# Performance work log

Measured on AMD Instinct MI355X. Metric: run time of the kernel, lower is better.

Reference implementation:

```python
import jax, jax.numpy as jnp
import numpy as np

N_NODES = 50000
N_EDGES = 800000
N_GRAPHS = 512
VOCAB = 128
HID = 64
NCLS = 5


def _seg_mean(vals, ids, num_segments):
    s = jax.ops.segment_sum(vals, ids, num_segments=num_segments)
    cnt = jax.ops.segment_sum(jnp.ones((vals.shape[0],), vals.dtype), ids, num_segments=num_segments)
    return s / jnp.maximum(cnt, 1.0)[:, None]


def sage_conv(x, src, dst, W_l, b_l, W_r):
    # PyG SAGEConv (mean aggr): out = lin_l(mean_{j in N(i)} x_j) + lin_r(x_i)
    agg = _seg_mean(x[src], dst, x.shape[0])          # [N, H] gather + scatter-mean
    return agg @ W_l.T + b_l + x @ W_r.T


def setup_inputs() -> dict:
    key = jax.random.key(0)
    ks = jax.random.split(key, 10)
    scale = 1.0 / np.sqrt(HID)
    x_tokens = jax.random.randint(ks[0], (N_NODES,), 0, VOCAB)
    edge_index = jax.random.randint(ks[1], (2, N_EDGES), 0, N_NODES)
    batch = jnp.sort(jax.random.randint(ks[2], (N_NODES,), 0, N_GRAPHS))
    return {
        "x_tokens": x_tokens,
        "edge_index": edge_index,
        "batch": batch,
        "embed": jax.random.normal(ks[3], (VOCAB, HID), jnp.float32),
        "W1l": jax.random.normal(ks[4], (HID, HID), jnp.float32) * scale,
        "b1l": jnp.zeros((HID,), jnp.float32),
        "W1r": jax.random.normal(ks[5], (HID, HID), jnp.float32) * scale,
        "W2l": jax.random.normal(ks[6], (HID, HID), jnp.float32) * scale,
        "b2l": jnp.zeros((HID,), jnp.float32),
        "W2r": jax.random.normal(ks[7], (HID, HID), jnp.float32) * scale,
        "Wlin": jax.random.normal(ks[8], (NCLS, HID), jnp.float32) * scale,
        "blin": jnp.zeros((NCLS,), jnp.float32),
    }


def reference(x_tokens, edge_index, batch, embed, W1l, b1l, W1r, W2l, b2l, W2r, Wlin, blin):
    src, dst = edge_index[0], edge_index[1]
    x = embed[x_tokens]                                  # [N, H] embedding lookup
    x = jax.nn.relu(sage_conv(x, src, dst, W1l, b1l, W1r))
    x = jax.nn.relu(sage_conv(x, src, dst, W2l, b2l, W2r))
    g = _seg_mean(x, batch, N_GRAPHS)                    # global_mean_pool -> [G, H]
    return g @ Wlin.T + blin                             # [G, num_classes]
```

## Files before the change

kernel.cpp:

```cpp
#include <hip/hip_runtime.h>

#define N_NODES  50000
#define N_EDGES  800000
#define N_GRAPHS 512
#define HID      64
#define NCLS     5
#define NB       64
#define EST      36
#define AST      68

typedef __attribute__((ext_vector_type(8))) short bf16x8;
typedef __attribute__((ext_vector_type(4))) float f32x4;

__device__ inline unsigned short f2bf(float f) {
    unsigned int u = __builtin_bit_cast(unsigned int, f);
    unsigned int r = (u + 0x7FFFu + ((u >> 16) & 1u)) >> 16;
    return (unsigned short)r;
}
__device__ inline unsigned int packbf(float a, float b) {
    return (unsigned int)f2bf(a) | ((unsigned int)f2bf(b) << 16);
}
__device__ inline float bf2f(unsigned int u16) {
    unsigned int t = u16 << 16;
    return __builtin_bit_cast(float, t);
}

#define XCDS   8
#define NPX    (N_NODES / XCDS)
#define ECHUNK ((N_EDGES + 255) / 256)
#define SEC_E  (ECHUNK * XCDS * 256)
#define EBUF_T (128 * 32)
#define PW_T   (64 * 64)
#define PREP_T (SEC_E + EBUF_T + N_NODES + 2 * PW_T)
__global__ void k_prep_fill(
    const int* __restrict__ src, const int* __restrict__ dst,
    const int* __restrict__ tok,
    int* __restrict__ cnt, unsigned int* __restrict__ bucket,
    const float* __restrict__ embed, unsigned int* __restrict__ ebufg,
    const int* __restrict__ batch,
    int* __restrict__ pos_start, int* __restrict__ pos_end,
    const float* __restrict__ W1l, const float* __restrict__ W1r,
    unsigned int* __restrict__ wb1,
    const float* __restrict__ W2l, const float* __restrict__ W2r,
    unsigned int* __restrict__ wb2) {
    int gid = blockIdx.x * blockDim.x + threadIdx.x;
    if (gid < SEC_E) {
        int blk   = gid >> 8;
        int range = blk & 7;
        int e     = (blk >> 3) * 256 + (gid & 255);
        if (e < N_EDGES) {
            int d = dst[e];
            int s = src[e];
            int lo = range * NPX;
            if (d >= lo && d < lo + NPX) {
                unsigned int t = (unsigned int)tok[s];
                int pos = atomicAdd(&cnt[d], 1);
                if (pos < NB) bucket[(long)d * NB + pos] = (unsigned int)s | (t << 16);
            }
        }
        return;
    }
    gid -= SEC_E;
    if (gid < EBUF_T) {
        int t = gid >> 5, c = gid & 31;
        float2 v = ((const float2*)(embed + (long)t * HID))[c];
        ebufg[gid] = packbf(v.x, v.y);
        return;
    }
    gid -= EBUF_T;
    if (gid < N_NODES) {
        int n = gid;
        int b = batch[n];
        if (n == 0 || batch[n - 1] != b) pos_start[b] = n;
        if (n == N_NODES - 1 || batch[n + 1] != b) pos_end[b] = n + 1;
        return;
    }
    gid -= N_NODES;
    if (gid < 2 * PW_T) {
        const float* Wl = (gid < PW_T) ? W1l : W2l;
        const float* Wr = (gid < PW_T) ? W1r : W2r;
        unsigned int* wb = (gid < PW_T) ? wb1 : wb2;
        int i = (gid < PW_T) ? gid : gid - PW_T;
        int h = i >> 6, c = i & 63;
        float2 v = (c < 32) ? ((const float2*)(Wl + (long)h * HID))[c]
                            : ((const float2*)(Wr + (long)h * HID))[c - 32];
        wb[i] = packbf(v.x, v.y);
    }
}

#define NPB 32
template <bool L1>
__global__ __launch_bounds__(512) void k_layer(
    const int* __restrict__ cnt, const unsigned int* __restrict__ bucket,
    const int* __restrict__ tok, const unsigned int* __restrict__ ebufg,
    const unsigned int* __restrict__ xb,
    const unsigned int* __restrict__ wb, const float* __restrict__ bl,
    unsigned short* __restrict__ xoutb)
{
    __shared__ unsigned int As[NPB * AST];
    __shared__ unsigned int elds[L1 ? 128 * EST : 1];
    const int tid  = threadIdx.x;
    const int wv   = tid >> 6;
    const int lane = tid & 63;
    const int n0   = blockIdx.x * NPB;

    if (L1) {
        for (int i = tid; i < EBUF_T; i += 512) {
            int t = i >> 5, c = i & 31;
            elds[t * EST + c] = ebufg[i];
        }
        __syncthreads();
    }

    const int q  = lane & 7;
    const int e8 = lane >> 3;

#pragma unroll
    for (int i = 0; i < 4; ++i) {
        int rl = wv * 4 + i;
        int nn = n0 + rl;
        int nc = min(nn, N_NODES - 1);
        int deg = cnt[nc];
        int m   = (nn < N_NODES) ? min(deg, NB) : 0;
        unsigned int v = (lane < m) ? bucket[(long)nc * NB + lane] : 0u;
        float f0 = 0, f1 = 0, f2 = 0, f3 = 0, f4 = 0, f5 = 0, f6 = 0, f7 = 0;
#pragma unroll
        for (int g = 0; g < 8; ++g) {
            int j = g * 8 + e8;
            unsigned int vv = __shfl(v, j, 64);
            if (j < m) {
                uint4 w4;
                if (L1) w4 = *(const uint4*)(elds + (vv >> 16) * EST + q * 4);
                else    w4 = *((const uint4*)(xb + (long)(vv & 0xffffu) * 32) + q);
                f0 += bf2f(w4.x & 0xffff); f1 += bf2f(w4.x >> 16);
                f2 += bf2f(w4.y & 0xffff); f3 += bf2f(w4.y >> 16);
                f4 += bf2f(w4.z & 0xffff); f5 += bf2f(w4.z >> 16);
                f6 += bf2f(w4.w & 0xffff); f7 += bf2f(w4.w >> 16);
            }
        }
#pragma unroll
        for (int o = 8; o < 64; o <<= 1) {
            f0 += __shfl_xor(f0, o, 64); f1 += __shfl_xor(f1, o, 64);
            f2 += __shfl_xor(f2, o, 64); f3 += __shfl_xor(f3, o, 64);
            f4 += __shfl_xor(f4, o, 64); f5 += __shfl_xor(f5, o, 64);
            f6 += __shfl_xor(f6, o, 64); f7 += __shfl_xor(f7, o, 64);
        }
        if (e8 == 0) {
            float inv = 1.0f / (float)max(deg, 1);
            uint4 o;
            o.x = packbf(f0 * inv, f1 * inv);
            o.y = packbf(f2 * inv, f3 * inv);
            o.z = packbf(f4 * inv, f5 * inv);
            o.w = packbf(f6 * inv, f7 * inv);
            *(uint4*)(As + rl * AST + q * 4) = o;
        } else if (e8 == 1) {
            uint4 sv;
            if (L1) { int tk = tok[nc]; sv = *(const uint4*)(elds + tk * EST + q * 4); }
            else    { sv = *((const uint4*)(xb + (long)nc * 32) + q); }
            *(uint4*)(As + rl * AST + 32 + q * 4) = sv;
        }
    }
    __syncthreads();

    const int s    = wv & 1;
    const int t    = wv >> 1;
    const int mm   = lane & 15;
    const int quad = lane >> 4;

    bf16x8 afr[4];
#pragma unroll
    for (int kst = 0; kst < 4; ++kst)
        afr[kst] = *(const bf16x8*)(As + (s * 16 + mm) * AST + kst * 16 + quad * 4);

    f32x4 acc = (f32x4){0.f, 0.f, 0.f, 0.f};
#pragma unroll
    for (int kst = 0; kst < 4; ++kst) {
        bf16x8 bfr = *(const bf16x8*)(wb + (t * 16 + mm) * 64 + kst * 16 + quad * 4);
        acc = __builtin_amdgcn_mfma_f32_16x16x32_bf16(bfr, afr[kst], acc, 0, 0, 0);
    }

    int node = n0 + s * 16 + mm;
    if (node < N_NODES) {
        int hb = t * 16 + quad * 4;
        float4 bb = *(const float4*)(bl + hb);
        ushort4 o;
        o.x = f2bf(fmaxf(acc[0] + bb.x, 0.f));
        o.y = f2bf(fmaxf(acc[1] + bb.y, 0.f));
        o.z = f2bf(fmaxf(acc[2] + bb.z, 0.f));
        o.w = f2bf(fmaxf(acc[3] + bb.w, 0.f));
        *(ushort4*)(xoutb + (long)node * HID + hb) = o;
    }
}

__global__ __launch_bounds__(256) void k_pool(
    const unsigned int* __restrict__ x2b,
    const int* __restrict__ pos_start, const int* __restrict__ pos_end,
    const float* __restrict__ Wlin, const float* __restrict__ blin,
    float* __restrict__ out)
{
    __shared__ float part[4][8][8];
    int g    = blockIdx.x;
    int tid  = threadIdx.x;
    int wv   = tid >> 6;
    int lane = tid & 63;
    int q    = lane & 7;
    int slot = wv * 8 + (lane >> 3);
    int s = pos_start[g], e = pos_end[g];
    float f0 = 0, f1 = 0, f2 = 0, f3 = 0, f4 = 0, f5 = 0, f6 = 0, f7 = 0;
    for (int n = s + slot; n < e; n += 32) {
        uint4 v = *((const uint4*)(x2b + (long)n * 32) + q);
        f0 += bf2f(v.x & 0xffff); f1 += bf2f(v.x >> 16);
        f2 += bf2f(v.y & 0xffff); f3 += bf2f(v.y >> 16);
        f4 += bf2f(v.z & 0xffff); f5 += bf2f(v.z >> 16);
        f6 += bf2f(v.w & 0xffff); f7 += bf2f(v.w >> 16);
    }
#pragma unroll
    for (int o = 8; o < 64; o <<= 1) {
        f0 += __shfl_xor(f0, o, 64); f1 += __shfl_xor(f1, o, 64);
        f2 += __shfl_xor(f2, o, 64); f3 += __shfl_xor(f3, o, 64);
        f4 += __shfl_xor(f4, o, 64); f5 += __shfl_xor(f5, o, 64);
        f6 += __shfl_xor(f6, o, 64); f7 += __shfl_xor(f7, o, 64);
    }
    if (lane < 8) {
        part[wv][lane][0] = f0; part[wv][lane][1] = f1;
        part[wv][lane][2] = f2; part[wv][lane][3] = f3;
        part[wv][lane][4] = f4; part[wv][lane][5] = f5;
        part[wv][lane][6] = f6; part[wv][lane][7] = f7;
    }
    __syncthreads();
    if (wv == 0) {
        f0 = part[0][q][0] + part[1][q][0] + part[2][q][0] + part[3][q][0];
        f1 = part[0][q][1] + part[1][q][1] + part[2][q][1] + part[3][q][1];
        f2 = part[0][q][2] + part[1][q][2] + part[2][q][2] + part[3][q][2];
        f3 = part[0][q][3] + part[1][q][3] + part[2][q][3] + part[3][q][3];
        f4 = part[0][q][4] + part[1][q][4] + part[2][q][4] + part[3][q][4];
        f5 = part[0][q][5] + part[1][q][5] + part[2][q][5] + part[3][q][5];
        f6 = part[0][q][6] + part[1][q][6] + part[2][q][6] + part[3][q][6];
        f7 = part[0][q][7] + part[1][q][7] + part[2][q][7] + part[3][q][7];
        float inv = 1.0f / (float)max(e - s, 1);
        f0 *= inv; f1 *= inv; f2 *= inv; f3 *= inv;
        f4 *= inv; f5 *= inv; f6 *= inv; f7 *= inv;
#pragma unroll
        for (int c = 0; c < NCLS; ++c) {
            const float* wr = Wlin + c * HID + q * 8;
            float p = f0 * wr[0] + f1 * wr[1] + f2 * wr[2] + f3 * wr[3] +
                      f4 * wr[4] + f5 * wr[5] + f6 * wr[6] + f7 * wr[7];
            p += __shfl_xor(p, 1, 64);
            p += __shfl_xor(p, 2, 64);
            p += __shfl_xor(p, 4, 64);
            if (lane == 0) out[g * NCLS + c] = p + blin[c];
        }
    }
}

extern "C" void kernel_launch(void* const* d_in, const int* in_sizes, int n_in,
                              void* d_out, int out_size, void* d_ws, size_t ws_size,
                              hipStream_t stream) {
    const int*   tok   = (const int*)d_in[0];
    const int*   eidx  = (const int*)d_in[1];
    const int*   batch = (const int*)d_in[2];
    const float* embed = (const float*)d_in[3];
    const float* W1l   = (const float*)d_in[4];
    const float* b1l   = (const float*)d_in[5];
    const float* W1r   = (const float*)d_in[6];
    const float* W2l   = (const float*)d_in[7];
    const float* b2l   = (const float*)d_in[8];
    const float* W2r   = (const float*)d_in[9];
    const float* Wlin  = (const float*)d_in[10];
    const float* blin  = (const float*)d_in[11];
    float* out = (float*)d_out;

    const int* src = eidx;
    const int* dst = eidx + N_EDGES;

    char* wsp = (char*)d_ws;
    size_t off = 0;
    auto alloc = [&](size_t bytes) -> void* {
        void* p = wsp + off;
        off = (off + bytes + 255) & ~(size_t)255;
        return p;
    };
    int*   cnt     = (int*)  alloc((size_t)N_NODES * 4);
    int*   pstart  = (int*)  alloc((size_t)N_GRAPHS * 4);
    int*   pend    = (int*)  alloc((size_t)N_GRAPHS * 4);
    unsigned int* bucket = (unsigned int*)alloc((size_t)N_NODES * NB * 4);
    unsigned int* x1b    = (unsigned int*)alloc((size_t)N_NODES * 32 * 4);
    unsigned int* x2b    = (unsigned int*)alloc((size_t)N_NODES * 32 * 4);
    unsigned int* ebufg  = (unsigned int*)alloc((size_t)128 * 32 * 4);
    unsigned int* wb1    = (unsigned int*)alloc((size_t)64 * 64 * 4);
    unsigned int* wb2    = (unsigned int*)alloc((size_t)64 * 64 * 4);

    hipMemsetAsync(cnt, 0, (char*)pend - (char*)cnt + (size_t)N_GRAPHS * 4, stream);

    k_prep_fill<<<(PREP_T + 255) / 256, 256, 0, stream>>>(
        src, dst, tok, cnt, bucket,
        embed, ebufg, batch, pstart, pend, W1l, W1r, wb1, W2l, W2r, wb2);

    const int LBLK = (N_NODES + NPB - 1) / NPB;
    k_layer<true><<<LBLK, 512, 0, stream>>>(cnt, bucket, tok, ebufg, nullptr,
                                            wb1, b1l, (unsigned short*)x1b);
    k_layer<false><<<LBLK, 512, 0, stream>>>(cnt, bucket, nullptr, nullptr, x1b,
                                             wb2, b2l, (unsigned short*)x2b);

    k_pool<<<N_GRAPHS, 256, 0, stream>>>(x2b, pstart, pend, Wlin, blin, out);
}
```

Baseline: 191.0 us.

## Fuse all stages into one persistent cooperative kernel with grid syncs

Replaces the memset, prep, two layer kernels and pool kernel with a single cooperative persistent kernel that uses grid.sync between phases, and keeps the multi-kernel path as a fallback if the cooperative launch fails. The aim is to remove launch gaps and tail effects between the small kernels. The edge bucketing drops the XCD-partitioned dst-range filter and scatters atomics directly. In exchange it pays for grid-wide barriers and limits the grid to resident blocks, and atomics are no longer localized per XCD.

Result: slower. 393.5 us (+106.0%).

```diff
diff --git a/kernel.cpp b/kernel.cpp
--- a/kernel.cpp
+++ b/kernel.cpp
@@ -1,4 +1,7 @@
 #include <hip/hip_runtime.h>
+#include <hip/hip_cooperative_groups.h>
+
+namespace cg = cooperative_groups;
 
 #define N_NODES  50000
 #define N_EDGES  800000
@@ -8,6 +11,10 @@
 #define NB       64
 #define EST      36
 #define AST      68
+#define NPB      32
+#define NGRP     ((N_NODES + NPB - 1) / NPB)
+#define EBUF_T   (128 * 32)
+#define PW_T     (64 * 64)
 
 typedef __attribute__((ext_vector_type(8))) short bf16x8;
 typedef __attribute__((ext_vector_type(4))) float f32x4;
@@ -25,14 +32,224 @@
     return __builtin_bit_cast(float, t);
 }
 
-#define XCDS   8
-#define NPX    (N_NODES / XCDS)
-#define ECHUNK ((N_EDGES + 255) / 256)
-#define SEC_E  (ECHUNK * XCDS * 256)
-#define EBUF_T (128 * 32)
-#define PW_T   (64 * 64)
-#define PREP_T (SEC_E + EBUF_T + N_NODES + 2 * PW_T)
-__global__ void k_prep_fill(
+struct KParams {
+    const int *src, *dst, *tok, *batch;
+    const float *embed, *W1l, *b1l, *W1r, *W2l, *b2l, *W2r, *Wlin, *blin;
+    int *cnt, *pstart, *pend;
+    unsigned int *bucket, *x1b, *x2b, *wb1, *wb2;
+    float *out;
+};
+
+__device__ __forceinline__ void layer_phase(
+    bool L1, const int* cnt, const unsigned int* bucket,
+    const int* tok, const unsigned int* xb,
+    const unsigned int* wb, const float* bl, unsigned short* xoutb,
+    unsigned int* As, const unsigned int* elds, int bid, int gsz, int tid)
+{
+    const int wv   = tid >> 6;
+    const int lane = tid & 63;
+    const int q    = lane & 7;
+    const int e8   = lane >> 3;
+
+    for (int grp = bid; grp < NGRP; grp += gsz) {
+        const int n0 = grp * NPB;
+#pragma unroll
+        for (int i = 0; i < 4; ++i) {
+            int rl = wv * 4 + i;
+            int nn = n0 + rl;
+            int nc = min(nn, N_NODES - 1);
+            int deg = cnt[nc];
+            int m   = (nn < N_NODES) ? min(deg, NB) : 0;
+            unsigned int v = (lane < m) ? bucket[(long)nc * NB + lane] : 0u;
+            float f0 = 0, f1 = 0, f2 = 0, f3 = 0, f4 = 0, f5 = 0, f6 = 0, f7 = 0;
+#pragma unroll
+            for (int g = 0; g < 8; ++g) {
+                int j = g * 8 + e8;
+                unsigned int vv = __shfl(v, j, 64);
+                if (j < m) {
+                    uint4 w4;
+                    if (L1) w4 = *(const uint4*)(elds + (vv >> 16) * EST + q * 4);
+                    else    w4 = *((const uint4*)(xb + (long)(vv & 0xffffu) * 32) + q);
+                    f0 += bf2f(w4.x & 0xffff); f1 += bf2f(w4.x >> 16);
+                    f2 += bf2f(w4.y & 0xffff); f3 += bf2f(w4.y >> 16);
+                    f4 += bf2f(w4.z & 0xffff); f5 += bf2f(w4.z >> 16);
+                    f6 += bf2f(w4.w & 0xffff); f7 += bf2f(w4.w >> 16);
+                }
+            }
+#pragma unroll
+            for (int o = 8; o < 64; o <<= 1) {
+                f0 += __shfl_xor(f0, o, 64); f1 += __shfl_xor(f1, o, 64);
+                f2 += __shfl_xor(f2, o, 64); f3 += __shfl_xor(f3, o, 64);
+                f4 += __shfl_xor(f4, o, 64); f5 += __shfl_xor(f5, o, 64);
+                f6 += __shfl_xor(f6, o, 64); f7 += __shfl_xor(f7, o, 64);
+            }
+            if (e8 == 0) {
+                float inv = 1.0f / (float)max(deg, 1);
+                uint4 o;
+                o.x = packbf(f0 * inv, f1 * inv);
+                o.y = packbf(f2 * inv, f3 * inv);
+                o.z = packbf(f4 * inv, f5 * inv);
+                o.w = packbf(f6 * inv, f7 * inv);
+                *(uint4*)(As + rl * AST + q * 4) = o;
+            } else if (e8 == 1) {
+                uint4 sv;
+                if (L1) { int tk = tok[nc]; sv = *(const uint4*)(elds + tk * EST + q * 4); }
+                else    { sv = *((const uint4*)(xb + (long)nc * 32) + q); }
+                *(uint4*)(As + rl * AST + 32 + q * 4) = sv;
+            }
+        }
+        __syncthreads();
+
+        const int s    = wv & 1;
+        const int t    = wv >> 1;
+        const int mm   = lane & 15;
+        const int quad = lane >> 4;
+
+        bf16x8 afr[4];
+#pragma unroll
+        for (int kst = 0; kst < 4; ++kst)
+            afr[kst] = *(const bf16x8*)(As + (s * 16 + mm) * AST + kst * 16 + quad * 4);
+
+        f32x4 acc = (f32x4){0.f, 0.f, 0.f, 0.f};
+#pragma unroll
+        for (int kst = 0; kst < 4; ++kst) {
+            bf16x8 bfr = *(const bf16x8*)(wb + (t * 16 + mm) * 64 + kst * 16 + quad * 4);
+            acc = __builtin_amdgcn_mfma_f32_16x16x32_bf16(bfr, afr[kst], acc, 0, 0, 0);
+        }
+
+        int node = n0 + s * 16 + mm;
+        if (node < N_NODES) {
+            int hb = t * 16 + quad * 4;
+            float4 bb = *(const float4*)(bl + hb);
+            ushort4 o;
+            o.x = f2bf(fmaxf(acc[0] + bb.x, 0.f));
+            o.y = f2bf(fmaxf(acc[1] + bb.y, 0.f));
+            o.z = f2bf(fmaxf(acc[2] + bb.z, 0.f));
+            o.w = f2bf(fmaxf(acc[3] + bb.w, 0.f));
+            *(ushort4*)(xoutb + (long)node * HID + hb) = o;
+        }
+        __syncthreads();
+    }
+}
+
+__global__ __launch_bounds__(512, 4) void k_all(KParams p)
+{
+    cg::grid_group grid = cg::this_grid();
+    __shared__ unsigned int elds[128 * EST];
+    __shared__ unsigned int As[NPB * AST];
+    __shared__ float part[8][8][8];
+
+    const int tid = threadIdx.x;
+    const int bid = blockIdx.x;
+    const int gsz = gridDim.x;
+    const int nth = gsz * 512;
+
+    for (int i = tid; i < EBUF_T; i += 512) {
+        int t = i >> 5, c = i & 31;
+        float2 v = ((const float2*)(p.embed + (long)t * HID))[c];
+        elds[t * EST + c] = packbf(v.x, v.y);
+    }
+    for (int g0 = bid * 512 + tid; g0 < N_NODES + 2 * N_GRAPHS + 2 * PW_T; g0 += nth) {
+        int g = g0;
+        if (g < N_NODES) { p.cnt[g] = 0; continue; }
+        g -= N_NODES;
+        if (g < N_GRAPHS) { p.pstart[g] = 0; continue; }
+        g -= N_GRAPHS;
+        if (g < N_GRAPHS) { p.pend[g] = 0; continue; }
+        g -= N_GRAPHS;
+        {
+            const float* Wl = (g < PW_T) ? p.W1l : p.W2l;
+            const float* Wr = (g < PW_T) ? p.W1r : p.W2r;
+            unsigned int* wb = (g < PW_T) ? p.wb1 : p.wb2;
+            int i = (g < PW_T) ? g : g - PW_T;
+            int h = i >> 6, c = i & 63;
+            float2 v = (c < 32) ? ((const float2*)(Wl + (long)h * HID))[c]
+                                : ((const float2*)(Wr + (long)h * HID))[c - 32];
+            wb[i] = packbf(v.x, v.y);
+        }
+    }
+    grid.sync();
+
+    for (int e = bid * 512 + tid; e < N_EDGES; e += nth) {
+        int d = p.dst[e];
+        int s = p.src[e];
+        unsigned int t = (unsigned int)p.tok[s];
+        int pos = atomicAdd(&p.cnt[d], 1);
+        if (pos < NB) p.bucket[(long)d * NB + pos] = (unsigned int)s | (t << 16);
+    }
+    for (int n = bid * 512 + tid; n < N_NODES; n += nth) {
+        int b = p.batch[n];
+        if (n == 0 || p.batch[n - 1] != b) p.pstart[b] = n;
+        if (n == N_NODES - 1 || p.batch[n + 1] != b) p.pend[b] = n + 1;
+    }
+    grid.sync();
+
+    layer_phase(true, p.cnt, p.bucket, p.tok, nullptr, p.wb1, p.b1l,
+                (unsigned short*)p.x1b, As, elds, bid, gsz, tid);
+    grid.sync();
+
+    layer_phase(false, p.cnt, p.bucket, nullptr, p.x1b, p.wb2, p.b2l,
+                (unsigned short*)p.x2b, As, elds, bid, gsz, tid);
+    grid.sync();
+
+    {
+        const int wv   = tid >> 6;
+        const int lane = tid & 63;
+        const int q    = lane & 7;
+        const int slot = wv * 8 + (lane >> 3);
+        for (int g = bid; g < N_GRAPHS; g += gsz) {
+            int s = p.pstart[g], e = p.pend[g];
+            float f0 = 0, f1 = 0, f2 = 0, f3 = 0, f4 = 0, f5 = 0, f6 = 0, f7 = 0;
+            for (int n = s + slot; n < e; n += 64) {
+                uint4 v = *((const uint4*)(p.x2b + (long)n * 32) + q);
+                f0 += bf2f(v.x & 0xffff); f1 += bf2f(v.x >> 16);
+                f2 += bf2f(v.y & 0xffff); f3 += bf2f(v.y >> 16);
+                f4 += bf2f(v.z & 0xffff); f5 += bf2f(v.z >> 16);
+                f6 += bf2f(v.w & 0xffff); f7 += bf2f(v.w >> 16);
+            }
+#pragma unroll
+            for (int o = 8; o < 64; o <<= 1) {
+                f0 += __shfl_xor(f0, o, 64); f1 += __shfl_xor(f1, o, 64);
+                f2 += __shfl_xor(f2, o, 64); f3 += __shfl_xor(f3, o, 64);
+                f4 += __shfl_xor(f4, o, 64); f5 += __shfl_xor(f5, o, 64);
+                f6 += __shfl_xor(f6, o, 64); f7 += __shfl_xor(f7, o, 64);
+            }
+            if (lane < 8) {
+                part[wv][lane][0] = f0; part[wv][lane][1] = f1;
+                part[wv][lane][2] = f2; part[wv][lane][3] = f3;
+                part[wv][lane][4] = f4; part[wv][lane][5] = f5;
+                part[wv][lane][6] = f6; part[wv][lane][7] = f7;
+            }
+            __syncthreads();
+            if (wv == 0) {
+                float s0 = 0, s1 = 0, s2 = 0, s3 = 0, s4 = 0, s5 = 0, s6 = 0, s7 = 0;
+#pragma unroll
+                for (int w = 0; w < 8; ++w) {
+                    s0 += part[w][q][0]; s1 += part[w][q][1];
+                    s2 += part[w][q][2]; s3 += part[w][q][3];
+                    s4 += part[w][q][4]; s5 += part[w][q][5];
+                    s6 += part[w][q][6]; s7 += part[w][q][7];
+                }
+                float inv = 1.0f / (float)max(e - s, 1);
+                s0 *= inv; s1 *= inv; s2 *= inv; s3 *= inv;
+                s4 *= inv; s5 *= inv; s6 *= inv; s7 *= inv;
+#pragma unroll
+                for (int c = 0; c < NCLS; ++c) {
+                    const float* wr = p.Wlin + c * HID + q * 8;
+                    float pr = s0 * wr[0] + s1 * wr[1] + s2 * wr[2] + s3 * wr[3] +
+                               s4 * wr[4] + s5 * wr[5] + s6 * wr[6] + s7 * wr[7];
+                    pr += __shfl_xor(pr, 1, 64);
+                    pr += __shfl_xor(pr, 2, 64);
+                    pr += __shfl_xor(pr, 4, 64);
+                    if (lane == 0) p.out[g * NCLS + c] = pr + p.blin[c];
+                }
+            }
+            __syncthreads();
+        }
+    }
+}
+
+__global__ void k_prep_fill_fb(
     const int* __restrict__ src, const int* __restrict__ dst,
     const int* __restrict__ tok,
     int* __restrict__ cnt, unsigned int* __restrict__ bucket,
@@ -44,23 +261,15 @@
     const float* __restrict__ W2l, const float* __restrict__ W2r,
     unsigned int* __restrict__ wb2) {
     int gid = blockIdx.x * blockDim.x + threadIdx.x;
-    if (gid < SEC_E) {
-        int blk   = gid >> 8;
-        int range = blk & 7;
-        int e     = (blk >> 3) * 256 + (gid & 255);
-        if (e < N_EDGES) {
-            int d = dst[e];
-            int s = src[e];
-            int lo = range * NPX;
-            if (d >= lo && d < lo + NPX) {
-                unsigned int t = (unsigned int)tok[s];
-                int pos = atomicAdd(&cnt[d], 1);
-                if (pos < NB) bucket[(long)d * NB + pos] = (unsigned int)s | (t << 16);
-            }
-        }
+    if (gid < N_EDGES) {
+        int d = dst[gid];
+        int s = src[gid];
+        unsigned int t = (unsigned int)tok[s];
+        int pos = atomicAdd(&cnt[d], 1);
+        if (pos < NB) bucket[(long)d * NB + pos] = (unsigned int)s | (t << 16);
         return;
     }
-    gid -= SEC_E;
+    gid -= N_EDGES;
     if (gid < EBUF_T) {
         int t = gid >> 5, c = gid & 31;
         float2 v = ((const float2*)(embed + (long)t * HID))[c];
@@ -88,9 +297,8 @@
     }
 }
 
-#define NPB 32
 template <bool L1>
-__global__ __launch_bounds__(512) void k_layer(
+__global__ __launch_bounds__(512) void k_layer_fb(
     const int* __restrict__ cnt, const unsigned int* __restrict__ bucket,
     const int* __restrict__ tok, const unsigned int* __restrict__ ebufg,
     const unsigned int* __restrict__ xb,
@@ -100,9 +308,7 @@
     __shared__ unsigned int As[NPB * AST];
     __shared__ unsigned int elds[L1 ? 128 * EST : 1];
     const int tid  = threadIdx.x;
-    const int wv   = tid >> 6;
-    const int lane = tid & 63;
-    const int n0   = blockIdx.x * NPB;
+    const int bid  = blockIdx.x;
 
     if (L1) {
         for (int i = tid; i < EBUF_T; i += 512) {
@@ -111,88 +317,10 @@
         }
         __syncthreads();
     }
-
-    const int q  = lane & 7;
-    const int e8 = lane >> 3;
-
-#pragma unroll
-    for (int i = 0; i < 4; ++i) {
-        int rl = wv * 4 + i;
-        int nn = n0 + rl;
-        int nc = min(nn, N_NODES - 1);
-        int deg = cnt[nc];
-        int m   = (nn < N_NODES) ? min(deg, NB) : 0;
-        unsigned int v = (lane < m) ? bucket[(long)nc * NB + lane] : 0u;
-        float f0 = 0, f1 = 0, f2 = 0, f3 = 0, f4 = 0, f5 = 0, f6 = 0, f7 = 0;
-#pragma unroll
-        for (int g = 0; g < 8; ++g) {
-            int j = g * 8 + e8;
-            unsigned int vv = __shfl(v, j, 64);
-            if (j < m) {
-                uint4 w4;
-                if (L1) w4 = *(const uint4*)(elds + (vv >> 16) * EST + q * 4);
-                else    w4 = *((const uint4*)(xb + (long)(vv & 0xffffu) * 32) + q);
-                f0 += bf2f(w4.x & 0xffff); f1 += bf2f(w4.x >> 16);
-                f2 += bf2f(w4.y & 0xffff); f3 += bf2f(w4.y >> 16);
-                f4 += bf2f(w4.z & 0xffff); f5 += bf2f(w4.z >> 16);
-                f6 += bf2f(w4.w & 0xffff); f7 += bf2f(w4.w >> 16);
-            }
-        }
-#pragma unroll
-        for (int o = 8; o < 64; o <<= 1) {
-            f0 += __shfl_xor(f0, o, 64); f1 += __shfl_xor(f1, o, 64);
-            f2 += __shfl_xor(f2, o, 64); f3 += __shfl_xor(f3, o, 64);
-            f4 += __shfl_xor(f4, o, 64); f5 += __shfl_xor(f5, o, 64);
-            f6 += __shfl_xor(f6, o, 64); f7 += __shfl_xor(f7, o, 64);
-        }
-        if (e8 == 0) {
-            float inv = 1.0f / (float)max(deg, 1);
-            uint4 o;
-            o.x = packbf(f0 * inv, f1 * inv);
-            o.y = packbf(f2 * inv, f3 * inv);
-            o.z = packbf(f4 * inv, f5 * inv);
-            o.w = packbf(f6 * inv, f7 * inv);
-            *(uint4*)(As + rl * AST + q * 4) = o;
-        } else if (e8 == 1) {
-            uint4 sv;
-            if (L1) { int tk = tok[nc]; sv = *(const uint4*)(elds + tk * EST + q * 4); }
-            else    { sv = *((const uint4*)(xb + (long)nc * 32) + q); }
-            *(uint4*)(As + rl * AST + 32 + q * 4) = sv;
-        }
-    }
-    __syncthreads();
-
-    const int s    = wv & 1;
-    const int t    = wv >> 1;
-    const int mm   = lane & 15;
-    const int quad = lane >> 4;
-
-    bf16x8 afr[4];
-#pragma unroll
-    for (int kst = 0; kst < 4; ++kst)
-        afr[kst] = *(const bf16x8*)(As + (s * 16 + mm) * AST + kst * 16 + quad * 4);
-
-    f32x4 acc = (f32x4){0.f, 0.f, 0.f, 0.f};
-#pragma unroll
-    for (int kst = 0; kst < 4; ++kst) {
-        bf16x8 bfr = *(const bf16x8*)(wb + (t * 16 + mm) * 64 + kst * 16 + quad * 4);
-        acc = __builtin_amdgcn_mfma_f32_16x16x32_bf16(bfr, afr[kst], acc, 0, 0, 0);
-    }
-
-    int node = n0 + s * 16 + mm;
-    if (node < N_NODES) {
-        int hb = t * 16 + quad * 4;
-        float4 bb = *(const float4*)(bl + hb);
-        ushort4 o;
-        o.x = f2bf(fmaxf(acc[0] + bb.x, 0.f));
-        o.y = f2bf(fmaxf(acc[1] + bb.y, 0.f));
-        o.z = f2bf(fmaxf(acc[2] + bb.z, 0.f));
-        o.w = f2bf(fmaxf(acc[3] + bb.w, 0.f));
-        *(ushort4*)(xoutb + (long)node * HID + hb) = o;
-    }
-}
-
-__global__ __launch_bounds__(256) void k_pool(
+    layer_phase(L1, cnt, bucket, tok, xb, wb, bl, xoutb, As, elds, bid, 1 << 30, tid);
+}
+
+__global__ __launch_bounds__(256) void k_pool_fb(
     const unsigned int* __restrict__ x2b,
     const int* __restrict__ pos_start, const int* __restrict__ pos_end,
     const float* __restrict__ Wlin, const float* __restrict__ blin,
@@ -290,17 +418,37 @@
     unsigned int* wb1    = (unsigned int*)alloc((size_t)64 * 64 * 4);
     unsigned int* wb2    = (unsigned int*)alloc((size_t)64 * 64 * 4);
 
+    KParams kp;
+    kp.src = src;   kp.dst = dst;   kp.tok = tok;   kp.batch = batch;
+    kp.embed = embed;
+    kp.W1l = W1l; kp.b1l = b1l; kp.W1r = W1r;
+    kp.W2l = W2l; kp.b2l = b2l; kp.W2r = W2r;
+    kp.Wlin = Wlin; kp.blin = blin;
+    kp.cnt = cnt; kp.pstart = pstart; kp.pend = pend;
+    kp.bucket = bucket; kp.x1b = x1b; kp.x2b = x2b;
+    kp.wb1 = wb1; kp.wb2 = wb2; kp.out = out;
+
+    static int bpc = 0;
+    if (bpc == 0) {
+        if (hipOccupancyMaxActiveBlocksPerMultiprocessor(&bpc, k_all, 512, 0) != hipSuccess || bpc < 1)
+            bpc = 2;
+    }
+    int grid = 256 * bpc;
+    if (grid > 1024) grid = 1024;
+
+    void* args[] = { (void*)&kp };
+    hipError_t err = hipLaunchCooperativeKernel((void*)k_all, dim3(grid), dim3(512),
+                                                args, 0, stream);
+    if (err == hipSuccess) return;
+
     hipMemsetAsync(cnt, 0, (char*)pend - (char*)cnt + (size_t)N_GRAPHS * 4, stream);
-
-    k_prep_fill<<<(PREP_T + 255) / 256, 256, 0, stream>>>(
+    int prep_t = N_EDGES + EBUF_T + N_NODES + 2 * PW_T;
+    k_prep_fill_fb<<<(prep_t + 255) / 256, 256, 0, stream>>>(
         src, dst, tok, cnt, bucket,
         embed, ebufg, batch, pstart, pend, W1l, W1r, wb1, W2l, W2r, wb2);
-
-    const int LBLK = (N_NODES + NPB - 1) / NPB;
-    k_layer<true><<<LBLK, 512, 0, stream>>>(cnt, bucket, tok, ebufg, nullptr,
-                                            wb1, b1l, (unsigned short*)x1b);
-    k_layer<false><<<LBLK, 512, 0, stream>>>(cnt, bucket, nullptr, nullptr, x1b,
-                                             wb2, b2l, (unsigned short*)x2b);
-
-    k_pool<<<N_GRAPHS, 256, 0, stream>>>(x2b, pstart, pend, Wlin, blin, out);
-}
+    k_layer_fb<true><<<NGRP, 512, 0, stream>>>(cnt, bucket, tok, ebufg, nullptr,
+                                               wb1, b1l, (unsigned short*)x1b);
+    k_layer_fb<false><<<NGRP, 512, 0, stream>>>(cnt, bucket, nullptr, nullptr, x1b,
+                                                wb2, b2l, (unsigned short*)x2b);
+    k_pool_fb<<<N_GRAPHS, 256, 0, stream>>>(x2b, pstart, pend, Wlin, blin, out);
+}
```
